# Optimization experiments

Hardware: AMD Instinct MI355X
Metric: run time of the kernel (lower is better)

## Reference

```python
import jax, jax.numpy as jnp
import numpy as np

N = 50000       # nodes
E = 1_600_000   # edges (avg degree 32)
LAT, HID, OUT = 64, 128, 64


def _add_self_loops(edge_index, edge_attr, n):
    loop = jnp.arange(n, dtype=edge_index.dtype)
    src = jnp.concatenate([edge_index[0], loop])
    dst = jnp.concatenate([edge_index[1], loop])
    ew = jnp.concatenate([edge_attr, jnp.ones((n,), edge_attr.dtype)])
    return src, dst, ew


def _gcn_conv(x, W, b, src, dst, ew, n):
    # x: [N, Fin] -> [N, Fout]; GCN: D^{-1/2}(A+I)D^{-1/2} X W + b
    h = x @ W                                             # [N, Fout]
    deg = jax.ops.segment_sum(ew, dst, num_segments=n)    # weighted in-degree
    dinv = jnp.where(deg > 0, jax.lax.rsqrt(deg), 0.0)
    norm = dinv[src] * ew * dinv[dst]                     # [E+N]
    out = jax.ops.segment_sum(norm[:, None] * h[src], dst, num_segments=n)
    return out + b


def setup_inputs() -> dict:
    key = jax.random.key(0)
    k = jax.random.split(key, 8)
    z = jax.random.normal(k[0], (N, LAT), jnp.float32)
    edge_index = jax.random.randint(k[1], (2, E), 0, N, dtype=jnp.int32)
    edge_attr = jax.random.uniform(k[2], (E,), jnp.float32)
    W1 = jax.random.normal(k[3], (LAT, HID), jnp.float32) / np.sqrt(LAT)
    b1 = jnp.zeros((HID,), jnp.float32)
    W2 = jax.random.normal(k[4], (HID, OUT), jnp.float32) / np.sqrt(HID)
    b2 = jnp.zeros((OUT,), jnp.float32)
    return {"z": z, "edge_index": edge_index, "edge_attr": edge_attr,
            "W1": W1, "b1": b1, "W2": W2, "b2": b2}


def reference(z, edge_index, edge_attr, W1, b1, W2, b2):
    n = z.shape[0]
    src, dst, ew = _add_self_loops(edge_index, edge_attr, n)
    hidden = jax.nn.relu(_gcn_conv(z, W1, b1, src, dst, ew, n))
    return _gcn_conv(hidden, W2, b2, src, dst, ew, n)
```

## Files before the change

kernel.cpp:

```cpp
#include <hip/hip_runtime.h>


#define NPB 128
#define CH  4096

typedef __attribute__((ext_vector_type(8))) short short8v;
typedef __attribute__((ext_vector_type(4))) float f32x4;

__device__ __forceinline__ float4 ld4(const float* p) {
    return *reinterpret_cast<const float4*>(p);
}

__device__ __forceinline__ unsigned bfr(float f) {
    unsigned u = __float_as_uint(f);
    return (u + 0x7FFFu + ((u >> 16) & 1u)) >> 16;
}
__device__ __forceinline__ void bf4(uint2 v, float& f0, float& f1, float& f2, float& f3) {
    f0 = __uint_as_float(v.x << 16);
    f1 = __uint_as_float(v.x & 0xFFFF0000u);
    f2 = __uint_as_float(v.y << 16);
    f3 = __uint_as_float(v.y & 0xFFFF0000u);
}

__global__ __launch_bounds__(256) void prep_kernel(const float* __restrict__ W1,
                                                   const float* __restrict__ W2,
                                                   unsigned short* __restrict__ W1T,
                                                   unsigned short* __restrict__ W2T) {
    for (int i = threadIdx.x; i < 128 * 64; i += 256) {
        int c = i >> 6, k = i & 63;
        W1T[i] = (unsigned short)bfr(W1[k * 128 + c]);
    }
    for (int i = threadIdx.x; i < 64 * 128; i += 256) {
        int c = i >> 7, k = i & 127;
        W2T[i] = (unsigned short)bfr(W2[k * 64 + c]);
    }
}

__global__ __launch_bounds__(256) void hist_kernel(const int* __restrict__ dst,
                                                   int* __restrict__ hist,
                                                   int E, int G1, int NBKT) {
    __shared__ int lh[512];
    for (int i = threadIdx.x; i < NBKT; i += 256) lh[i] = 0;
    __syncthreads();
    int g = blockIdx.x;
    int beg = g * CH, end = min(beg + CH, E);
    for (int j = beg + (int)threadIdx.x; j < end; j += 256)
        atomicAdd(&lh[dst[j] / NPB], 1);
    __syncthreads();
    for (int i = threadIdx.x; i < NBKT; i += 256) hist[(size_t)i * G1 + g] = lh[i];
}

__global__ __launch_bounds__(64) void bscan_kernel(int* __restrict__ hist,
                                                   int* __restrict__ btot, int G1) {
    int b = blockIdx.x;
    int* row = hist + (size_t)b * G1;
    int lane = threadIdx.x;
    int carry = 0;
    for (int g0 = 0; g0 < G1; g0 += 64) {
        int g = g0 + lane;
        int v = (g < G1) ? row[g] : 0;
        int incl = v;
#pragma unroll
        for (int off = 1; off < 64; off <<= 1) {
            int u = __shfl_up(incl, off, 64);
            if (lane >= off) incl += u;
        }
        if (g < G1) row[g] = carry + incl - v;
        carry += __shfl(incl, 63, 64);
    }
    if (lane == 0) btot[b] = carry;
}

__global__ __launch_bounds__(512) void tscan_kernel(const int* __restrict__ btot,
                                                    int* __restrict__ bbase, int NBKT) {
    __shared__ int ws[8];
    int t = threadIdx.x;
    int v = (t < NBKT) ? btot[t] : 0;
    int lane = t & 63, wid = t >> 6;
    int incl = v;
#pragma unroll
    for (int off = 1; off < 64; off <<= 1) {
        int u = __shfl_up(incl, off, 64);
        if (lane >= off) incl += u;
    }
    if (lane == 63) ws[wid] = incl;
    __syncthreads();
    int woff = 0;
#pragma unroll
    for (int w = 0; w < 8; ++w) if (w < wid) woff += ws[w];
    if (t < NBKT) bbase[t] = woff + incl - v;
}

__global__ __launch_bounds__(256) void scatter_kernel(const int* __restrict__ src,
                                                      const int* __restrict__ dst,
                                                      const float* __restrict__ ew,
                                                      const int* __restrict__ hist,
                                                      const int* __restrict__ bbase,
                                                      int2* __restrict__ tmp,
                                                      int E, int G1, int NBKT) {
    __shared__ int cursor[512];
    int g = blockIdx.x;
    for (int i = threadIdx.x; i < NBKT; i += 256)
        cursor[i] = bbase[i] + hist[(size_t)i * G1 + g];
    __syncthreads();
    int beg = g * CH, end = min(beg + CH, E);
    for (int j = beg + (int)threadIdx.x; j < end; j += 256) {
        int d = dst[j];
        int b = d / NPB;
        int pos = atomicAdd(&cursor[b], 1);
        tmp[pos] = make_int2(((d & (NPB - 1)) << 24) | src[j], __float_as_int(ew[j]));
    }
}

__global__ __launch_bounds__(256) void finalize_kernel(const int2* __restrict__ tmp,
                                                       const int* __restrict__ bbase,
                                                       const int* __restrict__ btot,
                                                       const float* __restrict__ z,
                                                       int* __restrict__ rowptr,
                                                       float* __restrict__ dinv,
                                                       int2* __restrict__ csr,
                                                       uint2* __restrict__ zs,
                                                       int n, int E) {
    __shared__ unsigned int hist[NPB];
    __shared__ float dvl[NPB];
    __shared__ int wsum_[2];
    int b = blockIdx.x;
    int base = bbase[b];
    int cnt  = btot[b];
    int tid  = threadIdx.x;
    if (tid < NPB) hist[tid] = 0;
    __syncthreads();
    for (int j = tid; j < cnt; j += 256) {
        int2 t = tmp[base + j];
        unsigned dlow = ((unsigned)t.x) >> 24;
        unsigned wfix = (unsigned)(__int_as_float(t.y) * 16384.0f);
        atomicAdd(&hist[dlow], (1u << 24) | wfix);
    }
    __syncthreads();
    int c = 0, incl = 0;
    unsigned pk = 0;
    if (tid < NPB) {
        pk = hist[tid];
        c = (int)(pk >> 24);
        incl = c;
#pragma unroll
        for (int off = 1; off < 64; off <<= 1) {
            int u = __shfl_up(incl, off, 64);
            if ((tid & 63) >= off) incl += u;
        }
        if ((tid & 63) == 63) wsum_[tid >> 6] = incl;
    }
    __syncthreads();
    if (tid < NPB) {
        int woff = (tid >= 64) ? wsum_[0] : 0;
        int excl = woff + incl - c;
        int node = b * NPB + tid;
        float dv = 0.f;
        if (node < n) {
            rowptr[node] = base + excl;
            float wdeg = (float)(pk & 0xFFFFFFu) * (1.0f / 16384.0f);
            dv = rsqrtf(wdeg + 1.0f);
            dinv[node] = dv;
        }
        dvl[tid]  = dv;
        hist[tid] = (unsigned)excl;
    }
    if (b == 0 && tid == 0) rowptr[n] = E;
    __syncthreads();
    for (int j = tid; j < cnt; j += 256) {
        int2 t = tmp[base + j];
        unsigned dlow = ((unsigned)t.x) >> 24;
        int srcv = t.x & 0xFFFFFF;
        int lr = (int)atomicAdd(&hist[dlow], 1u);
        csr[base + lr] = make_int2(srcv, t.y);
    }
    for (int t = tid; t < NPB * 16; t += 256) {
        int li = t >> 4;
        int node = b * NPB + li;
        if (node < n) {
            int k = t & 15;
            float dv = dvl[li];
            float4 f = ld4(z + (size_t)node * 64 + k * 4);
            zs[(size_t)node * 16 + k] =
                make_uint2(bfr(dv * f.x) | (bfr(dv * f.y) << 16),
                           bfr(dv * f.z) | (bfr(dv * f.w) << 16));
        }
    }
}

template<bool BIAS, bool OUTB>
__global__ __launch_bounds__(256) void gaggb_kernel(const int* __restrict__ rowptr,
                                                    const int2* __restrict__ csr,
                                                    const float* __restrict__ dinv,
                                                    const uint2* __restrict__ Hp,
                                                    const float* __restrict__ b,
                                                    void* __restrict__ out, int n) {
    int row  = (blockIdx.x * 256 + threadIdx.x) >> 6;
    int lane = threadIdx.x & 63;
    if (row >= n) return;
    int eg = lane >> 4, fq = lane & 15;
    int beg = rowptr[row], end = rowptr[row + 1];
    float dv = dinv[row];

    float ax = 0.f, ay = 0.f, az = 0.f, aw = 0.f;
    float f0, f1, f2, f3;
    int j = beg;
    for (; j + 16 <= end; j += 16) {
        int2 m0 = csr[j + eg];
        int2 m1 = csr[j + eg + 4];
        int2 m2 = csr[j + eg + 8];
        int2 m3 = csr[j + eg + 12];
        uint2 v0 = Hp[(size_t)(unsigned)(m0.x) * 16 + fq];
        uint2 v1 = Hp[(size_t)(unsigned)(m1.x) * 16 + fq];
        uint2 v2 = Hp[(size_t)(unsigned)(m2.x) * 16 + fq];
        uint2 v3 = Hp[(size_t)(unsigned)(m3.x) * 16 + fq];
        float w0 = __int_as_float(m0.y), w1 = __int_as_float(m1.y);
        float w2 = __int_as_float(m2.y), w3 = __int_as_float(m3.y);
        bf4(v0, f0, f1, f2, f3);
        ax += w0 * f0; ay += w0 * f1; az += w0 * f2; aw += w0 * f3;
        bf4(v1, f0, f1, f2, f3);
        ax += w1 * f0; ay += w1 * f1; az += w1 * f2; aw += w1 * f3;
        bf4(v2, f0, f1, f2, f3);
        ax += w2 * f0; ay += w2 * f1; az += w2 * f2; aw += w2 * f3;
        bf4(v3, f0, f1, f2, f3);
        ax += w3 * f0; ay += w3 * f1; az += w3 * f2; aw += w3 * f3;
    }
    for (; j + 4 <= end; j += 4) {
        int2 m0 = csr[j + eg];
        float w0 = __int_as_float(m0.y);
        uint2 v0 = Hp[(size_t)(unsigned)(m0.x) * 16 + fq];
        bf4(v0, f0, f1, f2, f3);
        ax += w0 * f0; ay += w0 * f1; az += w0 * f2; aw += w0 * f3;
    }
    if (j < end) {
        int idx = j + eg;
        if (idx < end) {
            int2 m0 = csr[idx];
            float w0 = __int_as_float(m0.y);
            uint2 v0 = Hp[(size_t)(unsigned)(m0.x) * 16 + fq];
            bf4(v0, f0, f1, f2, f3);
            ax += w0 * f0; ay += w0 * f1; az += w0 * f2; aw += w0 * f3;
        }
    }
    ax += __shfl_xor(ax, 16, 64); ay += __shfl_xor(ay, 16, 64);
    az += __shfl_xor(az, 16, 64); aw += __shfl_xor(aw, 16, 64);
    ax += __shfl_xor(ax, 32, 64); ay += __shfl_xor(ay, 32, 64);
    az += __shfl_xor(az, 32, 64); aw += __shfl_xor(aw, 32, 64);

    if (eg == 0) {
        uint2 sv = Hp[(size_t)row * 16 + fq];
        float s0, s1, s2, s3;
        bf4(sv, s0, s1, s2, s3);
        float4 o;
        o.x = dv * (ax + s0);
        o.y = dv * (ay + s1);
        o.z = dv * (az + s2);
        o.w = dv * (aw + s3);
        if (BIAS) {
            float4 bb = ld4(b + fq * 4);
            o.x += bb.x; o.y += bb.y; o.z += bb.z; o.w += bb.w;
        }
        if (OUTB) {
            uint2 pv = make_uint2(bfr(o.x) | (bfr(o.y) << 16),
                                  bfr(o.z) | (bfr(o.w) << 16));
            reinterpret_cast<uint2*>(out)[(size_t)row * 16 + fq] = pv;
        } else {
            reinterpret_cast<float4*>(out)[(size_t)row * 16 + fq] = o;
        }
    }
}

__global__ __launch_bounds__(256) void densemfma_kernel(
        const unsigned short* __restrict__ t1b,
        const unsigned short* __restrict__ W1T,
        const float* __restrict__ b1,
        const unsigned short* __restrict__ W2T,
        const float* __restrict__ dinv,
        unsigned short* __restrict__ hs,
        int n) {
    __shared__ __align__(16) unsigned short hT[4][16][136];
    int wv = threadIdx.x >> 6;
    int l  = threadIdx.x & 63;
    int m  = l & 15, g = l >> 4;
    int R  = blockIdx.x * 64 + wv * 16;

    short8v a0 = {0,0,0,0,0,0,0,0}, a1 = {0,0,0,0,0,0,0,0};
    int rowA = R + m;
    if (rowA < n) {
        a0 = *reinterpret_cast<const short8v*>(t1b + (size_t)rowA * 64 + 8 * g);
        a1 = *reinterpret_cast<const short8v*>(t1b + (size_t)rowA * 64 + 32 + 8 * g);
    }
#pragma unroll
    for (int ct = 0; ct < 8; ++ct) {
        const unsigned short* wp = W1T + (size_t)(ct * 16 + m) * 64 + 8 * g;
        short8v wb0 = *reinterpret_cast<const short8v*>(wp);
        short8v wb1 = *reinterpret_cast<const short8v*>(wp + 32);
        f32x4 c = {0.f, 0.f, 0.f, 0.f};
        c = __builtin_amdgcn_mfma_f32_16x16x32_bf16(a0, wb0, c, 0, 0, 0);
        c = __builtin_amdgcn_mfma_f32_16x16x32_bf16(a1, wb1, c, 0, 0, 0);
        float bb = b1[ct * 16 + m];
#pragma unroll
        for (int r = 0; r < 4; ++r) {
            float v = fmaxf(c[r] + bb, 0.f);
            hT[wv][4 * g + r][ct * 16 + m] = (unsigned short)bfr(v);
        }
    }
    __syncthreads();

    f32x4 acc2[4];
#pragma unroll
    for (int ct = 0; ct < 4; ++ct) acc2[ct] = (f32x4){0.f, 0.f, 0.f, 0.f};
#pragma unroll
    for (int kk = 0; kk < 4; ++kk) {
        short8v ha = *reinterpret_cast<const short8v*>(&hT[wv][m][kk * 32 + 8 * g]);
#pragma unroll
        for (int ct = 0; ct < 4; ++ct) {
            short8v wb = *reinterpret_cast<const short8v*>(
                W2T + (size_t)(ct * 16 + m) * 128 + kk * 32 + 8 * g);
            acc2[ct] = __builtin_amdgcn_mfma_f32_16x16x32_bf16(ha, wb, acc2[ct], 0, 0, 0);
        }
    }
    __syncthreads();

#pragma unroll
    for (int r = 0; r < 4; ++r) {
        int grow = R + 4 * g + r;
        float dv = (grow < n) ? dinv[grow] : 0.f;
#pragma unroll
        for (int ct = 0; ct < 4; ++ct)
            hT[wv][4 * g + r][ct * 16 + m] = (unsigned short)bfr(acc2[ct][r] * dv);
    }
    __syncthreads();
    int growO = R + m;
    if (growO < n) {
        uint4 u0 = *reinterpret_cast<const uint4*>(&hT[wv][m][g * 16]);
        uint4 u1 = *reinterpret_cast<const uint4*>(&hT[wv][m][g * 16 + 8]);
        *reinterpret_cast<uint4*>(hs + (size_t)growO * 64 + g * 16) = u0;
        *reinterpret_cast<uint4*>(hs + (size_t)growO * 64 + g * 16 + 8) = u1;
    }
}

extern "C" void kernel_launch(void* const* d_in, const int* in_sizes, int n_in,
                              void* d_out, int out_size, void* d_ws, size_t ws_size,
                              hipStream_t stream) {
    const float* z  = (const float*)d_in[0];
    const int*   ei = (const int*)d_in[1];
    const float* ea = (const float*)d_in[2];
    const float* W1 = (const float*)d_in[3];
    const float* b1 = (const float*)d_in[4];
    const float* W2 = (const float*)d_in[5];
    const float* b2 = (const float*)d_in[6];
    float* out = (float*)d_out;

    const int n = in_sizes[0] / 64;
    const int E = in_sizes[2];
    const int* src = ei;
    const int* dst = ei + E;
    const int NBKT = (n + NPB - 1) / NPB;
    const int G1   = (E + CH - 1) / CH;

    float* ws = (float*)d_ws;
    size_t p = 0;
    auto alloc = [&](size_t elems) { size_t o = p; p += (elems + 63) & ~63ull; return o; };
    float* dinv   = ws + alloc(n);
    int*   rowptr = (int*)(ws + alloc((size_t)n + 1));
    int*   btot   = (int*)(ws + alloc(NBKT));
    int*   bbase  = (int*)(ws + alloc(NBKT));
    int2*  csr    = (int2*)(ws + alloc((size_t)E * 2));
    unsigned short* t1b = (unsigned short*)(ws + alloc((size_t)n * 32));
    uint2* zs     = (uint2*)(ws + alloc((size_t)n * 32));
    unsigned short* W1T = (unsigned short*)(ws + alloc(4096));
    unsigned short* W2T = (unsigned short*)(ws + alloc(4096));
    float* X      = ws + alloc((size_t)E * 2 + (size_t)NBKT * G1 + 64);
    int2*  tmp    = (int2*)X;
    int*   hist   = (int*)(X + (size_t)E * 2);
    (void)ws_size;

    prep_kernel<<<1, 256, 0, stream>>>(W1, W2, W1T, W2T);
    hist_kernel<<<G1, 256, 0, stream>>>(dst, hist, E, G1, NBKT);
    bscan_kernel<<<NBKT, 64, 0, stream>>>(hist, btot, G1);
    tscan_kernel<<<1, 512, 0, stream>>>(btot, bbase, NBKT);
    scatter_kernel<<<G1, 256, 0, stream>>>(src, dst, ea, hist, bbase, tmp, E, G1, NBKT);
    finalize_kernel<<<NBKT, 256, 0, stream>>>(tmp, bbase, btot, z, rowptr, dinv,
                                              csr, zs, n, E);

    const int gblocks = (n + 3) / 4;
    gaggb_kernel<false, true><<<gblocks, 256, 0, stream>>>(rowptr, csr, dinv, zs,
                                                           nullptr, t1b, n);
    densemfma_kernel<<<(n + 63) / 64, 256, 0, stream>>>(t1b, W1T, b1, W2T, dinv,
                                                        (unsigned short*)zs, n);
    gaggb_kernel<true, false><<<gblocks, 256, 0, stream>>>(rowptr, csr, dinv, zs,
                                                           b2, out, n);
}
```

Before: 158.2 us.

## Fold bucket scan and weight prep into consumer kernels; persistent dense MFMA kernel

Removes the separate weight-transpose and bucket-total scan launches by recomputing the small scan inside each scatter/finalize block and converting weights into LDS inside the dense MFMA kernel. The dense kernel becomes a grid-stride persistent kernel with 256 blocks and drops unneeded block barriers. The aggregation kernel gains a 32-edge unrolled loop for more memory-level parallelism. This trades launch overhead for redundant per-block scan and weight conversion work.

```diff
diff --git a/kernel.cpp b/kernel.cpp
--- a/kernel.cpp
+++ b/kernel.cpp
@@ -22,18 +22,28 @@
     f3 = __uint_as_float(v.y & 0xFFFF0000u);
 }
 
-__global__ __launch_bounds__(256) void prep_kernel(const float* __restrict__ W1,
-                                                   const float* __restrict__ W2,
-                                                   unsigned short* __restrict__ W1T,
-                                                   unsigned short* __restrict__ W2T) {
-    for (int i = threadIdx.x; i < 128 * 64; i += 256) {
-        int c = i >> 6, k = i & 63;
-        W1T[i] = (unsigned short)bfr(W1[k * 128 + c]);
-    }
-    for (int i = threadIdx.x; i < 64 * 128; i += 256) {
-        int c = i >> 7, k = i & 127;
-        W2T[i] = (unsigned short)bfr(W2[k * 64 + c]);
-    }
+__device__ __forceinline__ void scan_btot(const int* __restrict__ btot, int NBKT,
+                                          int* bbs, int* wtot) {
+    int tid = threadIdx.x;
+    int v0 = (2 * tid     < NBKT) ? btot[2 * tid]     : 0;
+    int v1 = (2 * tid + 1 < NBKT) ? btot[2 * tid + 1] : 0;
+    int s = v0 + v1;
+    int lane = tid & 63, wid = tid >> 6;
+    int incl = s;
+#pragma unroll
+    for (int off = 1; off < 64; off <<= 1) {
+        int u = __shfl_up(incl, off, 64);
+        if (lane >= off) incl += u;
+    }
+    if (lane == 63) wtot[wid] = incl;
+    __syncthreads();
+    int woff = 0;
+#pragma unroll
+    for (int w = 0; w < 4; ++w) if (w < wid) woff += wtot[w];
+    int ex = woff + incl - s;
+    if (2 * tid     < NBKT) bbs[2 * tid]     = ex;
+    if (2 * tid + 1 < NBKT) bbs[2 * tid + 1] = ex + v0;
+    __syncthreads();
 }
 
 __global__ __launch_bounds__(256) void hist_kernel(const int* __restrict__ dst,
@@ -71,37 +81,20 @@
     if (lane == 0) btot[b] = carry;
 }
 
-__global__ __launch_bounds__(512) void tscan_kernel(const int* __restrict__ btot,
-                                                    int* __restrict__ bbase, int NBKT) {
-    __shared__ int ws[8];
-    int t = threadIdx.x;
-    int v = (t < NBKT) ? btot[t] : 0;
-    int lane = t & 63, wid = t >> 6;
-    int incl = v;
-#pragma unroll
-    for (int off = 1; off < 64; off <<= 1) {
-        int u = __shfl_up(incl, off, 64);
-        if (lane >= off) incl += u;
-    }
-    if (lane == 63) ws[wid] = incl;
-    __syncthreads();
-    int woff = 0;
-#pragma unroll
-    for (int w = 0; w < 8; ++w) if (w < wid) woff += ws[w];
-    if (t < NBKT) bbase[t] = woff + incl - v;
-}
-
 __global__ __launch_bounds__(256) void scatter_kernel(const int* __restrict__ src,
                                                       const int* __restrict__ dst,
                                                       const float* __restrict__ ew,
                                                       const int* __restrict__ hist,
-                                                      const int* __restrict__ bbase,
+                                                      const int* __restrict__ btot,
                                                       int2* __restrict__ tmp,
                                                       int E, int G1, int NBKT) {
+    __shared__ int bbs[512];
+    __shared__ int wtot[4];
     __shared__ int cursor[512];
+    scan_btot(btot, NBKT, bbs, wtot);
     int g = blockIdx.x;
     for (int i = threadIdx.x; i < NBKT; i += 256)
-        cursor[i] = bbase[i] + hist[(size_t)i * G1 + g];
+        cursor[i] = bbs[i] + hist[(size_t)i * G1 + g];
     __syncthreads();
     int beg = g * CH, end = min(beg + CH, E);
     for (int j = beg + (int)threadIdx.x; j < end; j += 256) {
@@ -113,19 +106,20 @@
 }
 
 __global__ __launch_bounds__(256) void finalize_kernel(const int2* __restrict__ tmp,
-                                                       const int* __restrict__ bbase,
                                                        const int* __restrict__ btot,
                                                        const float* __restrict__ z,
                                                        int* __restrict__ rowptr,
                                                        float* __restrict__ dinv,
                                                        int2* __restrict__ csr,
                                                        uint2* __restrict__ zs,
-                                                       int n, int E) {
+                                                       int n, int E, int NBKT) {
+    __shared__ int bbs[512];
+    __shared__ int wsum_[4];
     __shared__ unsigned int hist[NPB];
     __shared__ float dvl[NPB];
-    __shared__ int wsum_[2];
+    scan_btot(btot, NBKT, bbs, wsum_);
     int b = blockIdx.x;
-    int base = bbase[b];
+    int base = bbs[b];
     int cnt  = btot[b];
     int tid  = threadIdx.x;
     if (tid < NPB) hist[tid] = 0;
@@ -205,6 +199,44 @@
     float ax = 0.f, ay = 0.f, az = 0.f, aw = 0.f;
     float f0, f1, f2, f3;
     int j = beg;
+    for (; j + 32 <= end; j += 32) {
+        int2 m0 = csr[j + eg];
+        int2 m1 = csr[j + eg + 4];
+        int2 m2 = csr[j + eg + 8];
+        int2 m3 = csr[j + eg + 12];
+        int2 m4 = csr[j + eg + 16];
+        int2 m5 = csr[j + eg + 20];
+        int2 m6 = csr[j + eg + 24];
+        int2 m7 = csr[j + eg + 28];
+        uint2 v0 = Hp[(size_t)(unsigned)(m0.x) * 16 + fq];
+        uint2 v1 = Hp[(size_t)(unsigned)(m1.x) * 16 + fq];
+        uint2 v2 = Hp[(size_t)(unsigned)(m2.x) * 16 + fq];
+        uint2 v3 = Hp[(size_t)(unsigned)(m3.x) * 16 + fq];
+        uint2 v4 = Hp[(size_t)(unsigned)(m4.x) * 16 + fq];
+        uint2 v5 = Hp[(size_t)(unsigned)(m5.x) * 16 + fq];
+        uint2 v6 = Hp[(size_t)(unsigned)(m6.x) * 16 + fq];
+        uint2 v7 = Hp[(size_t)(unsigned)(m7.x) * 16 + fq];
+        float w0 = __int_as_float(m0.y), w1 = __int_as_float(m1.y);
+        float w2 = __int_as_float(m2.y), w3 = __int_as_float(m3.y);
+        float w4 = __int_as_float(m4.y), w5 = __int_as_float(m5.y);
+        float w6 = __int_as_float(m6.y), w7 = __int_as_float(m7.y);
+        bf4(v0, f0, f1, f2, f3);
+        ax += w0 * f0; ay += w0 * f1; az += w0 * f2; aw += w0 * f3;
+        bf4(v1, f0, f1, f2, f3);
+        ax += w1 * f0; ay += w1 * f1; az += w1 * f2; aw += w1 * f3;
+        bf4(v2, f0, f1, f2, f3);
+        ax += w2 * f0; ay += w2 * f1; az += w2 * f2; aw += w2 * f3;
+        bf4(v3, f0, f1, f2, f3);
+        ax += w3 * f0; ay += w3 * f1; az += w3 * f2; aw += w3 * f3;
+        bf4(v4, f0, f1, f2, f3);
+        ax += w4 * f0; ay += w4 * f1; az += w4 * f2; aw += w4 * f3;
+        bf4(v5, f0, f1, f2, f3);
+        ax += w5 * f0; ay += w5 * f1; az += w5 * f2; aw += w5 * f3;
+        bf4(v6, f0, f1, f2, f3);
+        ax += w6 * f0; ay += w6 * f1; az += w6 * f2; aw += w6 * f3;
+        bf4(v7, f0, f1, f2, f3);
+        ax += w7 * f0; ay += w7 * f1; az += w7 * f2; aw += w7 * f3;
+    }
     for (; j + 16 <= end; j += 16) {
         int2 m0 = csr[j + eg];
         int2 m1 = csr[j + eg + 4];
@@ -272,71 +304,81 @@
 
 __global__ __launch_bounds__(256) void densemfma_kernel(
         const unsigned short* __restrict__ t1b,
-        const unsigned short* __restrict__ W1T,
+        const float* __restrict__ W1,
         const float* __restrict__ b1,
-        const unsigned short* __restrict__ W2T,
+        const float* __restrict__ W2,
         const float* __restrict__ dinv,
         unsigned short* __restrict__ hs,
         int n) {
+    __shared__ __align__(16) unsigned short W1s[128][68];
+    __shared__ __align__(16) unsigned short W2s[64][132];
+    __shared__ float b1s[128];
     __shared__ __align__(16) unsigned short hT[4][16][136];
+    for (int i = threadIdx.x; i < 128 * 64; i += 256) {
+        int c = i >> 6, k = i & 63;
+        W1s[c][k] = (unsigned short)bfr(W1[k * 128 + c]);
+    }
+    for (int i = threadIdx.x; i < 64 * 128; i += 256) {
+        int c = i >> 7, k = i & 127;
+        W2s[c][k] = (unsigned short)bfr(W2[k * 64 + c]);
+    }
+    if (threadIdx.x < 128) b1s[threadIdx.x] = b1[threadIdx.x];
+    __syncthreads();
+
     int wv = threadIdx.x >> 6;
     int l  = threadIdx.x & 63;
     int m  = l & 15, g = l >> 4;
-    int R  = blockIdx.x * 64 + wv * 16;
-
-    short8v a0 = {0,0,0,0,0,0,0,0}, a1 = {0,0,0,0,0,0,0,0};
-    int rowA = R + m;
-    if (rowA < n) {
-        a0 = *reinterpret_cast<const short8v*>(t1b + (size_t)rowA * 64 + 8 * g);
-        a1 = *reinterpret_cast<const short8v*>(t1b + (size_t)rowA * 64 + 32 + 8 * g);
-    }
-#pragma unroll
-    for (int ct = 0; ct < 8; ++ct) {
-        const unsigned short* wp = W1T + (size_t)(ct * 16 + m) * 64 + 8 * g;
-        short8v wb0 = *reinterpret_cast<const short8v*>(wp);
-        short8v wb1 = *reinterpret_cast<const short8v*>(wp + 32);
-        f32x4 c = {0.f, 0.f, 0.f, 0.f};
-        c = __builtin_amdgcn_mfma_f32_16x16x32_bf16(a0, wb0, c, 0, 0, 0);
-        c = __builtin_amdgcn_mfma_f32_16x16x32_bf16(a1, wb1, c, 0, 0, 0);
-        float bb = b1[ct * 16 + m];
+    int ngrp = (n + 63) >> 6;
+    for (int grp = blockIdx.x; grp < ngrp; grp += gridDim.x) {
+        int R = grp * 64 + wv * 16;
+        short8v a0 = {0,0,0,0,0,0,0,0}, a1 = {0,0,0,0,0,0,0,0};
+        int rowA = R + m;
+        if (rowA < n) {
+            a0 = *reinterpret_cast<const short8v*>(t1b + (size_t)rowA * 64 + 8 * g);
+            a1 = *reinterpret_cast<const short8v*>(t1b + (size_t)rowA * 64 + 32 + 8 * g);
+        }
+#pragma unroll
+        for (int ct = 0; ct < 8; ++ct) {
+            short8v wb0 = *reinterpret_cast<const short8v*>(&W1s[ct * 16 + m][8 * g]);
+            short8v wb1 = *reinterpret_cast<const short8v*>(&W1s[ct * 16 + m][32 + 8 * g]);
+            f32x4 c = {0.f, 0.f, 0.f, 0.f};
+            c = __builtin_amdgcn_mfma_f32_16x16x32_bf16(a0, wb0, c, 0, 0, 0);
+            c = __builtin_amdgcn_mfma_f32_16x16x32_bf16(a1, wb1, c, 0, 0, 0);
+            float bb = b1s[ct * 16 + m];
+#pragma unroll
+            for (int r = 0; r < 4; ++r) {
+                float v = fmaxf(c[r] + bb, 0.f);
+                hT[wv][4 * g + r][ct * 16 + m] = (unsigned short)bfr(v);
+            }
+        }
+        f32x4 acc2[4];
+#pragma unroll
+        for (int ct = 0; ct < 4; ++ct) acc2[ct] = (f32x4){0.f, 0.f, 0.f, 0.f};
+#pragma unroll
+        for (int kk = 0; kk < 4; ++kk) {
+            short8v ha = *reinterpret_cast<const short8v*>(&hT[wv][m][kk * 32 + 8 * g]);
+#pragma unroll
+            for (int ct = 0; ct < 4; ++ct) {
+                short8v wb = *reinterpret_cast<const short8v*>(
+                    &W2s[ct * 16 + m][kk * 32 + 8 * g]);
+                acc2[ct] = __builtin_amdgcn_mfma_f32_16x16x32_bf16(ha, wb, acc2[ct], 0, 0, 0);
+            }
+        }
 #pragma unroll
         for (int r = 0; r < 4; ++r) {
-            float v = fmaxf(c[r] + bb, 0.f);
-            hT[wv][4 * g + r][ct * 16 + m] = (unsigned short)bfr(v);
-        }
-    }
-    __syncthreads();
-
-    f32x4 acc2[4];
-#pragma unroll
-    for (int ct = 0; ct < 4; ++ct) acc2[ct] = (f32x4){0.f, 0.f, 0.f, 0.f};
-#pragma unroll
-    for (int kk = 0; kk < 4; ++kk) {
-        short8v ha = *reinterpret_cast<const short8v*>(&hT[wv][m][kk * 32 + 8 * g]);
-#pragma unroll
-        for (int ct = 0; ct < 4; ++ct) {
-            short8v wb = *reinterpret_cast<const short8v*>(
-                W2T + (size_t)(ct * 16 + m) * 128 + kk * 32 + 8 * g);
-            acc2[ct] = __builtin_amdgcn_mfma_f32_16x16x32_bf16(ha, wb, acc2[ct], 0, 0, 0);
-        }
-    }
-    __syncthreads();
-
-#pragma unroll
-    for (int r = 0; r < 4; ++r) {
-        int grow = R + 4 * g + r;
-        float dv = (grow < n) ? dinv[grow] : 0.f;
-#pragma unroll
-        for (int ct = 0; ct < 4; ++ct)
-            hT[wv][4 * g + r][ct * 16 + m] = (unsigned short)bfr(acc2[ct][r] * dv);
-    }
-    __syncthreads();
-    int growO = R + m;
-    if (growO < n) {
-        uint4 u0 = *reinterpret_cast<const uint4*>(&hT[wv][m][g * 16]);
-        uint4 u1 = *reinterpret_cast<const uint4*>(&hT[wv][m][g * 16 + 8]);
-        *reinterpret_cast<uint4*>(hs + (size_t)growO * 64 + g * 16) = u0;
-        *reinterpret_cast<uint4*>(hs + (size_t)growO * 64 + g * 16 + 8) = u1;
+            int grow = R + 4 * g + r;
+            float dv = (grow < n) ? dinv[grow] : 0.f;
+#pragma unroll
+            for (int ct = 0; ct < 4; ++ct)
+                hT[wv][4 * g + r][ct * 16 + m] = (unsigned short)bfr(acc2[ct][r] * dv);
+        }
+        int growO = R + m;
+        if (growO < n) {
+            uint4 u0 = *reinterpret_cast<const uint4*>(&hT[wv][m][g * 16]);
+            uint4 u1 = *reinterpret_cast<const uint4*>(&hT[wv][m][g * 16 + 8]);
+            *reinterpret_cast<uint4*>(hs + (size_t)growO * 64 + g * 16) = u0;
+            *reinterpret_cast<uint4*>(hs + (size_t)growO * 64 + g * 16 + 8) = u1;
+        }
     }
 }
 
@@ -365,30 +407,25 @@
     float* dinv   = ws + alloc(n);
     int*   rowptr = (int*)(ws + alloc((size_t)n + 1));
     int*   btot   = (int*)(ws + alloc(NBKT));
-    int*   bbase  = (int*)(ws + alloc(NBKT));
     int2*  csr    = (int2*)(ws + alloc((size_t)E * 2));
     unsigned short* t1b = (unsigned short*)(ws + alloc((size_t)n * 32));
     uint2* zs     = (uint2*)(ws + alloc((size_t)n * 32));
-    unsigned short* W1T = (unsigned short*)(ws + alloc(4096));
-    unsigned short* W2T = (unsigned short*)(ws + alloc(4096));
     float* X      = ws + alloc((size_t)E * 2 + (size_t)NBKT * G1 + 64);
     int2*  tmp    = (int2*)X;
     int*   hist   = (int*)(X + (size_t)E * 2);
     (void)ws_size;
 
-    prep_kernel<<<1, 256, 0, stream>>>(W1, W2, W1T, W2T);
     hist_kernel<<<G1, 256, 0, stream>>>(dst, hist, E, G1, NBKT);
     bscan_kernel<<<NBKT, 64, 0, stream>>>(hist, btot, G1);
-    tscan_kernel<<<1, 512, 0, stream>>>(btot, bbase, NBKT);
-    scatter_kernel<<<G1, 256, 0, stream>>>(src, dst, ea, hist, bbase, tmp, E, G1, NBKT);
-    finalize_kernel<<<NBKT, 256, 0, stream>>>(tmp, bbase, btot, z, rowptr, dinv,
-                                              csr, zs, n, E);
+    scatter_kernel<<<G1, 256, 0, stream>>>(src, dst, ea, hist, btot, tmp, E, G1, NBKT);
+    finalize_kernel<<<NBKT, 256, 0, stream>>>(tmp, btot, z, rowptr, dinv,
+                                              csr, zs, n, E, NBKT);
 
     const int gblocks = (n + 3) / 4;
     gaggb_kernel<false, true><<<gblocks, 256, 0, stream>>>(rowptr, csr, dinv, zs,
                                                            nullptr, t1b, n);
-    densemfma_kernel<<<(n + 63) / 64, 256, 0, stream>>>(t1b, W1T, b1, W2T, dinv,
-                                                        (unsigned short*)zs, n);
+    densemfma_kernel<<<256, 256, 0, stream>>>(t1b, W1, b1, W2, dinv,
+                                              (unsigned short*)zs, n);
     gaggb_kernel<true, false><<<gblocks, 256, 0, stream>>>(rowptr, csr, dinv, zs,
                                                            b2, out, n);
 }
```

Measured after the change: 149.6 us. 1.06x faster.
